# Kernel optimization log

Measured on AMD Instinct MI355X. Metric: run time of the kernel, lower is better.

Reference implementation:

```python
import jax, jax.numpy as jnp
import numpy as np

B, S, H, D, V = 256, 128, 1024, 256, 1858


def setup_inputs() -> dict:
    key = jax.random.key(0)
    ks = jax.random.split(key, 13)
    s = 1.0 / np.sqrt(H)
    return {
        "hidden_states": jax.random.normal(ks[0], (B, S, H), jnp.float32),
        "Wf": jax.random.normal(ks[1], (D, H), jnp.float32) * s,
        "bf": jax.random.normal(ks[2], (D,), jnp.float32) * 0.01,
        "Wt": jax.random.normal(ks[3], (D, H), jnp.float32) * s,
        "bt": jax.random.normal(ks[4], (D,), jnp.float32) * 0.01,
        "Wg": jax.random.normal(ks[5], (D, H), jnp.float32) * s,
        "bg": jax.random.normal(ks[6], (D,), jnp.float32) * 0.01,
        "promo_tab": jax.random.normal(ks[7], (5, D), jnp.float32),
        "Ws": jax.random.normal(ks[8], (1, D), jnp.float32) * (1.0 / np.sqrt(D)),
        "bs": jax.random.normal(ks[9], (1,), jnp.float32) * 0.01,
        "from_sqs": jax.random.randint(ks[10], (V,), 0, 64, jnp.int32),
        "to_sqs": jax.random.randint(ks[11], (V,), 0, 64, jnp.int32),
        "promo_types": jax.random.randint(ks[12], (V,), 0, 5, jnp.int32),
    }


def reference(hidden_states, Wf, bf, Wt, bt, Wg, bg, promo_tab, Ws, bs,
              from_sqs, to_sqs, promo_types):
    # hidden_states: [B, S, H]; squares are tokens 3:67, global token is 0.
    sq_hidden = hidden_states[:, 3:67, :]          # [B, 64, H]
    global_hidden = hidden_states[:, 0, :]         # [B, H]

    # Linear commutes with gather: project the 64 unique squares first,
    # then gather per move (same math as gather-then-project).
    fp = jnp.einsum('bsh,dh->bsd', sq_hidden, Wf) + bf   # [B, 64, D]
    tp = jnp.einsum('bsh,dh->bsd', sq_hidden, Wt) + bt   # [B, 64, D]
    gp = global_hidden @ Wg.T + bg                       # [B, D]

    from_proj = fp[:, from_sqs, :]                       # [B, V, D]
    to_proj = tp[:, to_sqs, :]                           # [B, V, D]
    promo_feats = promo_tab[promo_types]                 # [V, D]

    combined = from_proj * to_proj + gp[:, None, :] + promo_feats[None]
    # score_proj: Linear(D, 1), then squeeze(-1) -> [B, V]
    return jnp.einsum('bvd,d->bv', jax.nn.relu(combined), Ws[0]) + bs[0]
```

## Files before the change

kernel.cpp:

```cpp
#include <hip/hip_runtime.h>

#define NB   256
#define NSQ  64
#define NH   1024
#define ND   256
#define NV   1858
#define M_   (NB * NSQ)
#define N_   512
#define NKT  32

typedef __attribute__((ext_vector_type(4))) float f32x4;
typedef __attribute__((ext_vector_type(8))) short bf16x8;
typedef __attribute__((ext_vector_type(8))) unsigned short u16x8;

__device__ __forceinline__ unsigned short bf16_rne(float x) {
    unsigned u = __float_as_uint(x);
    unsigned r = u + 0x7fffu + ((u >> 16) & 1u);
    return (unsigned short)(r >> 16);
}

__device__ __forceinline__ void gload16(const void* g, void* l) {
    __builtin_amdgcn_global_load_lds(
        (const __attribute__((address_space(1))) unsigned int*)g,
        (__attribute__((address_space(3))) unsigned int*)l, 16, 0, 0);
}

__device__ __forceinline__ void split8(const float4 a, const float4 b,
                                       u16x8& hi, u16x8& lo) {
    float vv[8] = {a.x, a.y, a.z, a.w, b.x, b.y, b.z, b.w};
#pragma unroll
    for (int j = 0; j < 8; ++j) {
        unsigned short hb = bf16_rne(vv[j]);
        hi[j] = hb;
        lo[j] = bf16_rne(vv[j] - __uint_as_float((unsigned)hb << 16));
    }
}

__global__ __launch_bounds__(256) void cast_W_kernel(
    const float* __restrict__ Wf, const float* __restrict__ Wt,
    char* __restrict__ Whi, char* __restrict__ Wlo) {
    int bid = blockIdx.x;
    int tid = threadIdx.x;
    int o = tid * 16;
    int g_l = o >> 10;
    int w = o & 1023;
    int s = w >> 8;
    int r = (w >> 4) & 15;
    int nrb = bid >> 5, kt = bid & 31;
    int n = nrb * 64 + g_l * 16 + r;
    int k = kt * 32 + s * 8;
    const float* src = ((n < ND) ? (Wf + (size_t)n * NH) : (Wt + (size_t)(n - ND) * NH)) + k;
    size_t outb = ((size_t)((nrb >> 1) * 32 + kt) << 13) + ((nrb & 1) << 12) + o;
    float4 v0 = ((const float4*)src)[0];
    float4 v1 = ((const float4*)src)[1];
    u16x8 h, l;
    split8(v0, v1, h, l);
    *(u16x8*)(Whi + outb) = h;
    *(u16x8*)(Wlo + outb) = l;
}

__global__ __launch_bounds__(1024) void gp_kernel(
    const float* __restrict__ hid, const float* __restrict__ Wg,
    const float* __restrict__ bg, float* __restrict__ gp) {
    __shared__ float h[NH];
    int b = blockIdx.x;
    int tid = threadIdx.x;
    if (tid < 256) ((float4*)h)[tid] = ((const float4*)(hid + (size_t)b * 128 * NH))[tid];
    __syncthreads();
    int wave = tid >> 6, lane = tid & 63;
    const float4* hs = (const float4*)h;
    for (int dd = 0; dd < 16; ++dd) {
        int d = wave * 16 + dd;
        const float4* wrow = (const float4*)(Wg + (size_t)d * NH);
        float acc = 0.f;
#pragma unroll
        for (int p = 0; p < 4; ++p) {
            float4 w = wrow[p * 64 + lane];
            float4 x = hs[p * 64 + lane];
            acc += w.x * x.x + w.y * x.y + w.z * x.z + w.w * x.w;
        }
#pragma unroll
        for (int o = 32; o > 0; o >>= 1) acc += __shfl_xor(acc, o, 64);
        if (lane == 0) gp[(size_t)b * ND + d] = acc + bg[d];
    }
}

__global__ __launch_bounds__(256) void gemm3f_kernel(
    const float* __restrict__ hid,
    const char* __restrict__ Whi, const char* __restrict__ Wlo,
    const float* __restrict__ bfv, const float* __restrict__ btv,
    float* __restrict__ C) {
    __shared__ __align__(16) char lA[16384];
    __shared__ __align__(16) char lB[16384];
    int tid = threadIdx.x;
    int lane = tid & 63, wv = tid >> 6;
    int wgid = (blockIdx.x & 7) * 64 + (blockIdx.x >> 3);
    int nt = wgid & 3;
    int mt = wgid >> 2;
    int wm = (wv >> 1) * 64, wn = (wv & 1) * 64;
    int fr = lane & 15, kh = lane >> 4;

    int r = tid >> 1, h = tid & 1;
    const float* asrc = hid +
        (size_t)((2 * mt + (r >> 6)) * 128 + 3 + (r & 63)) * NH + h * 16;
    int awb = (r >> 4) * 1024 + h * 512 + (r & 15) * 16;

    const char* bsrch = Whi + ((size_t)(nt * NKT) << 13) + tid * 16;
    const char* bsrcl = Wlo + ((size_t)(nt * NKT) << 13) + tid * 16;

    f32x4 acc[4][4] = {};
    float4 va0, va1, va2, va3, vn0, vn1, vn2, vn3;
    va0 = ((const float4*)asrc)[0];
    va1 = ((const float4*)asrc)[1];
    va2 = ((const float4*)asrc)[2];
    va3 = ((const float4*)asrc)[3];

    for (int kt = 0; kt < NKT; ++kt) {
        size_t tb = (size_t)kt << 13;
        gload16(bsrch + tb, lB + tid * 16);
        gload16(bsrch + tb + 4096, lB + 4096 + tid * 16);
        gload16(bsrcl + tb, lB + 8192 + tid * 16);
        gload16(bsrcl + tb + 4096, lB + 12288 + tid * 16);

        u16x8 h0, h1, l0, l1;
        split8(va0, va1, h0, l0);
        split8(va2, va3, h1, l1);
        *(u16x8*)(lA + awb) = h0;
        *(u16x8*)(lA + awb + 256) = h1;
        *(u16x8*)(lA + 8192 + awb) = l0;
        *(u16x8*)(lA + 8192 + awb + 256) = l1;
        __syncthreads();

        int ktn = (kt + 1) & (NKT - 1);
        const float* an = asrc + ktn * 32;
        vn0 = ((const float4*)an)[0];
        vn1 = ((const float4*)an)[1];
        vn2 = ((const float4*)an)[2];
        vn3 = ((const float4*)an)[3];

        bf16x8 ah[4], al[4], bh[4], bl[4];
#pragma unroll
        for (int f = 0; f < 4; ++f) {
            int ea = (wm + f * 16) * 64 + kh * 256 + fr * 16;
            int eb = (wn + f * 16) * 64 + kh * 256 + fr * 16;
            ah[f] = *(const bf16x8*)(lA + ea);
            al[f] = *(const bf16x8*)(lA + 8192 + ea);
            bh[f] = *(const bf16x8*)(lB + eb);
            bl[f] = *(const bf16x8*)(lB + 8192 + eb);
        }
#pragma unroll
        for (int i = 0; i < 4; ++i)
#pragma unroll
            for (int j = 0; j < 4; ++j) {
                acc[i][j] = __builtin_amdgcn_mfma_f32_16x16x32_bf16(ah[i], bh[j], acc[i][j], 0, 0, 0);
                acc[i][j] = __builtin_amdgcn_mfma_f32_16x16x32_bf16(ah[i], bl[j], acc[i][j], 0, 0, 0);
                acc[i][j] = __builtin_amdgcn_mfma_f32_16x16x32_bf16(al[i], bh[j], acc[i][j], 0, 0, 0);
            }
        __syncthreads();
        va0 = vn0; va1 = vn1; va2 = vn2; va3 = vn3;
    }

    const float* bias = (nt < 2) ? bfv : btv;
    int nb0 = nt * 128 - ((nt < 2) ? 0 : 256);
#pragma unroll
    for (int j = 0; j < 4; ++j) {
        int ncol = nt * 128 + wn + j * 16 + fr;
        float bv = bias[nb0 + wn + j * 16 + fr];
#pragma unroll
        for (int i = 0; i < 4; ++i) {
            int mrow = mt * 128 + wm + i * 16 + kh * 4;
#pragma unroll
            for (int rr = 0; rr < 4; ++rr) {
                C[(size_t)(mrow + rr) * N_ + ncol] = acc[i][j][rr] + bv;
            }
        }
    }
}

__global__ __launch_bounds__(1024) void out_kernel(
    const float* __restrict__ C, const float* __restrict__ gp,
    const float* __restrict__ promo_tab, const float* __restrict__ Wsv,
    const float* __restrict__ bsv,
    const int* __restrict__ from_sqs, const int* __restrict__ to_sqs,
    const int* __restrict__ ptypes, float* __restrict__ out) {
    __shared__ float cb[NSQ * N_];
    __shared__ float gpl[ND];
    __shared__ float wsl[ND];
    __shared__ float pl[5 * ND];
    __shared__ int fsq[NV], tsq[NV], pty[NV];
    int b = blockIdx.x;
    int tid = threadIdx.x;
    const float4* src = (const float4*)(C + (size_t)b * NSQ * N_);
    float4* dst = (float4*)cb;
#pragma unroll
    for (int i = 0; i < 8; ++i) dst[tid + i * 1024] = src[tid + i * 1024];
    if (tid < 64) ((float4*)gpl)[tid] = ((const float4*)(gp + (size_t)b * ND))[tid];
    else if (tid < 128) ((float4*)wsl)[tid - 64] = ((const float4*)Wsv)[tid - 64];
    else if (tid < 448) ((float4*)pl)[tid - 128] = ((const float4*)promo_tab)[tid - 128];
    for (int v = tid; v < NV; v += 1024) {
        fsq[v] = from_sqs[v];
        tsq[v] = to_sqs[v];
        pty[v] = ptypes[v];
    }
    __syncthreads();

    int wave = tid >> 6, lane = tid & 63;
    float bias0 = bsv[0];
    const float4* cb4 = (const float4*)cb;
    const float4* gp4 = (const float4*)gpl;
    const float4* ws4 = (const float4*)wsl;
    const float4* pl4 = (const float4*)pl;
    for (int v = wave; v < NV; v += 16) {
        int sf = fsq[v];
        int st = tsq[v];
        int p  = pty[v];
        float4 a = cb4[sf * 128 + lane];
        float4 t = cb4[st * 128 + 64 + lane];
        float4 g = gp4[lane];
        float4 pp = pl4[p * 64 + lane];
        float4 w = ws4[lane];
        float c0 = a.x * t.x + g.x + pp.x;
        float c1 = a.y * t.y + g.y + pp.y;
        float c2 = a.z * t.z + g.z + pp.z;
        float c3 = a.w * t.w + g.w + pp.w;
        float s = fmaxf(c0, 0.f) * w.x + fmaxf(c1, 0.f) * w.y +
                  fmaxf(c2, 0.f) * w.z + fmaxf(c3, 0.f) * w.w;
#pragma unroll
        for (int o = 32; o > 0; o >>= 1) s += __shfl_xor(s, o, 64);
        if (lane == 0) out[(size_t)b * NV + v] = s + bias0;
    }
}

extern "C" void kernel_launch(void* const* d_in, const int* in_sizes, int n_in,
                              void* d_out, int out_size, void* d_ws, size_t ws_size,
                              hipStream_t stream) {
    (void)in_sizes; (void)n_in; (void)out_size; (void)ws_size;
    const float* hid   = (const float*)d_in[0];
    const float* Wf    = (const float*)d_in[1];
    const float* bfv   = (const float*)d_in[2];
    const float* Wt    = (const float*)d_in[3];
    const float* btv   = (const float*)d_in[4];
    const float* Wg    = (const float*)d_in[5];
    const float* bgv   = (const float*)d_in[6];
    const float* promo = (const float*)d_in[7];
    const float* Wsv   = (const float*)d_in[8];
    const float* bsv   = (const float*)d_in[9];
    const int* from_sqs = (const int*)d_in[10];
    const int* to_sqs   = (const int*)d_in[11];
    const int* ptypes   = (const int*)d_in[12];
    float* out = (float*)d_out;

    char* ws = (char*)d_ws;
    char* Whi = ws;
    char* Wlo = ws + 1048576;
    float* C  = (float*)(ws + 2097152);
    float* gp = (float*)(ws + 35651584);

    cast_W_kernel<<<256, 256, 0, stream>>>(Wf, Wt, Whi, Wlo);
    gp_kernel<<<256, 1024, 0, stream>>>(hid, Wg, bgv, gp);
    gemm3f_kernel<<<512, 256, 0, stream>>>(hid, Whi, Wlo, bfv, btv, C);
    out_kernel<<<256, 1024, 0, stream>>>(C, gp, promo, Wsv, bsv,
                                         from_sqs, to_sqs, ptypes, out);
}
```

Before: 328.7 us.

## Double-buffer LDS tiles in split-bf16 GEMM to overlap loads with MFMA

Converts the projection GEMM main loop to a two-stage LDS ping-pong. The next tile's B loads and A split-writes are issued before the current tile's MFMAs, cutting the two barriers per k-step down to one. This is meant to hide global-to-LDS latency behind compute. In exchange LDS use doubles to 64KB per block, which may lower occupancy, and the loop issues wrapped redundant prefetches on the final iterations.

```diff
diff --git a/kernel.cpp b/kernel.cpp
--- a/kernel.cpp
+++ b/kernel.cpp
@@ -90,14 +90,13 @@
     const char* __restrict__ Whi, const char* __restrict__ Wlo,
     const float* __restrict__ bfv, const float* __restrict__ btv,
     float* __restrict__ C) {
-    __shared__ __align__(16) char lA[16384];
-    __shared__ __align__(16) char lB[16384];
+    __shared__ __align__(16) char lA[32768];
+    __shared__ __align__(16) char lB[32768];
     int tid = threadIdx.x;
     int lane = tid & 63, wv = tid >> 6;
     int wgid = (blockIdx.x & 7) * 64 + (blockIdx.x >> 3);
     int nt = wgid & 3;
     int mt = wgid >> 2;
-    int wm = (wv >> 1) * 64, wn = (wv & 1) * 64;
     int fr = lane & 15, kh = lane >> 4;
 
     int r = tid >> 1, h = tid & 1;
@@ -108,58 +107,80 @@
     const char* bsrch = Whi + ((size_t)(nt * NKT) << 13) + tid * 16;
     const char* bsrcl = Wlo + ((size_t)(nt * NKT) << 13) + tid * 16;
 
+    int afro = (wv >> 1) * 4096 + kh * 256 + fr * 16;
+    int bfro = (wv & 1) * 4096 + kh * 256 + fr * 16;
+
+#define BSTG(ktn, p)                                                      \
+    do {                                                                  \
+        size_t tb = (size_t)(ktn) << 13;                                  \
+        gload16(bsrch + tb,        lB + (p) * 16384 + tid * 16);          \
+        gload16(bsrch + tb + 4096, lB + (p) * 16384 + 4096 + tid * 16);   \
+        gload16(bsrcl + tb,        lB + (p) * 16384 + 8192 + tid * 16);   \
+        gload16(bsrcl + tb + 4096, lB + (p) * 16384 + 12288 + tid * 16);  \
+    } while (0)
+
+#define ASPLIT(v0, v1, v2, v3, p)                                         \
+    do {                                                                  \
+        u16x8 h0, h1, l0, l1;                                             \
+        split8(v0, v1, h0, l0);                                           \
+        split8(v2, v3, h1, l1);                                           \
+        *(u16x8*)(lA + (p) * 16384 + awb) = h0;                           \
+        *(u16x8*)(lA + (p) * 16384 + awb + 256) = h1;                     \
+        *(u16x8*)(lA + (p) * 16384 + 8192 + awb) = l0;                    \
+        *(u16x8*)(lA + (p) * 16384 + 8192 + awb + 256) = l1;              \
+    } while (0)
+
+#define ALOAD(d0, d1, d2, d3, ktn)                                        \
+    do {                                                                  \
+        const float* ap = asrc + (size_t)(ktn) * 32;                      \
+        d0 = ((const float4*)ap)[0];                                      \
+        d1 = ((const float4*)ap)[1];                                      \
+        d2 = ((const float4*)ap)[2];                                      \
+        d3 = ((const float4*)ap)[3];                                      \
+    } while (0)
+
+#define FRAG_MFMA(p)                                                      \
+    do {                                                                  \
+        bf16x8 ah[4], al[4], bh[4], bl[4];                                \
+        _Pragma("unroll") for (int f = 0; f < 4; ++f) {                   \
+            ah[f] = *(const bf16x8*)(lA + (p) * 16384 + afro + f * 1024); \
+            al[f] = *(const bf16x8*)(lA + (p) * 16384 + 8192 + afro + f * 1024); \
+            bh[f] = *(const bf16x8*)(lB + (p) * 16384 + bfro + f * 1024); \
+            bl[f] = *(const bf16x8*)(lB + (p) * 16384 + 8192 + bfro + f * 1024); \
+        }                                                                 \
+        _Pragma("unroll") for (int i = 0; i < 4; ++i)                     \
+            _Pragma("unroll") for (int j = 0; j < 4; ++j) {               \
+                acc[i][j] = __builtin_amdgcn_mfma_f32_16x16x32_bf16(ah[i], bh[j], acc[i][j], 0, 0, 0); \
+                acc[i][j] = __builtin_amdgcn_mfma_f32_16x16x32_bf16(ah[i], bl[j], acc[i][j], 0, 0, 0); \
+                acc[i][j] = __builtin_amdgcn_mfma_f32_16x16x32_bf16(al[i], bh[j], acc[i][j], 0, 0, 0); \
+            }                                                             \
+    } while (0)
+
     f32x4 acc[4][4] = {};
-    float4 va0, va1, va2, va3, vn0, vn1, vn2, vn3;
-    va0 = ((const float4*)asrc)[0];
-    va1 = ((const float4*)asrc)[1];
-    va2 = ((const float4*)asrc)[2];
-    va3 = ((const float4*)asrc)[3];
-
-    for (int kt = 0; kt < NKT; ++kt) {
-        size_t tb = (size_t)kt << 13;
-        gload16(bsrch + tb, lB + tid * 16);
-        gload16(bsrch + tb + 4096, lB + 4096 + tid * 16);
-        gload16(bsrcl + tb, lB + 8192 + tid * 16);
-        gload16(bsrcl + tb + 4096, lB + 12288 + tid * 16);
-
-        u16x8 h0, h1, l0, l1;
-        split8(va0, va1, h0, l0);
-        split8(va2, va3, h1, l1);
-        *(u16x8*)(lA + awb) = h0;
-        *(u16x8*)(lA + awb + 256) = h1;
-        *(u16x8*)(lA + 8192 + awb) = l0;
-        *(u16x8*)(lA + 8192 + awb + 256) = l1;
+    float4 a00, a01, a02, a03, a10, a11, a12, a13;
+
+    BSTG(0, 0);
+    ALOAD(a00, a01, a02, a03, 0);
+    ALOAD(a10, a11, a12, a13, 1);
+    ASPLIT(a00, a01, a02, a03, 0);
+    __syncthreads();
+
+#pragma unroll 1
+    for (int tt = 0; tt < 16; ++tt) {
+        int t0 = 2 * tt;
+        BSTG((t0 + 1) & 31, 1);
+        ASPLIT(a10, a11, a12, a13, 1);
+        ALOAD(a00, a01, a02, a03, (t0 + 2) & 31);
+        FRAG_MFMA(0);
         __syncthreads();
-
-        int ktn = (kt + 1) & (NKT - 1);
-        const float* an = asrc + ktn * 32;
-        vn0 = ((const float4*)an)[0];
-        vn1 = ((const float4*)an)[1];
-        vn2 = ((const float4*)an)[2];
-        vn3 = ((const float4*)an)[3];
-
-        bf16x8 ah[4], al[4], bh[4], bl[4];
-#pragma unroll
-        for (int f = 0; f < 4; ++f) {
-            int ea = (wm + f * 16) * 64 + kh * 256 + fr * 16;
-            int eb = (wn + f * 16) * 64 + kh * 256 + fr * 16;
-            ah[f] = *(const bf16x8*)(lA + ea);
-            al[f] = *(const bf16x8*)(lA + 8192 + ea);
-            bh[f] = *(const bf16x8*)(lB + eb);
-            bl[f] = *(const bf16x8*)(lB + 8192 + eb);
-        }
-#pragma unroll
-        for (int i = 0; i < 4; ++i)
-#pragma unroll
-            for (int j = 0; j < 4; ++j) {
-                acc[i][j] = __builtin_amdgcn_mfma_f32_16x16x32_bf16(ah[i], bh[j], acc[i][j], 0, 0, 0);
-                acc[i][j] = __builtin_amdgcn_mfma_f32_16x16x32_bf16(ah[i], bl[j], acc[i][j], 0, 0, 0);
-                acc[i][j] = __builtin_amdgcn_mfma_f32_16x16x32_bf16(al[i], bh[j], acc[i][j], 0, 0, 0);
-            }
+        BSTG((t0 + 2) & 31, 0);
+        ASPLIT(a00, a01, a02, a03, 0);
+        ALOAD(a10, a11, a12, a13, (t0 + 3) & 31);
+        FRAG_MFMA(1);
         __syncthreads();
-        va0 = vn0; va1 = vn1; va2 = vn2; va3 = vn3;
-    }
-
+    }
+
+    int wm = (wv >> 1) * 64, wn = (wv & 1) * 64;
     const float* bias = (nt < 2) ? bfv : btv;
     int nb0 = nt * 128 - ((nt < 2) ? 0 : 256);
 #pragma unroll
@@ -175,6 +196,10 @@
             }
         }
     }
+#undef BSTG
+#undef ASPLIT
+#undef ALOAD
+#undef FRAG_MFMA
 }
 
 __global__ __launch_bounds__(1024) void out_kernel(
```

Result: faster. 320.9 us (-2.4%).
